# Kernel tuning notes

Measured on AMD Instinct MI355X. Metric: run time of the kernel, lower is better.

Reference implementation:

```python
import jax, jax.numpy as jnp
import numpy as np

B, D, NH, HD, L, P, FF = 2, 256, 8, 32, 4, 4, 1024
SPATIAL = np.array([[100, 100], [50, 50], [25, 25], [13, 13]], dtype=np.int64)
S_TOTAL = int(SPATIAL.prod(1).sum())  # 13294
EPS = 1e-5


def setup_inputs() -> dict:
    key = jax.random.key(0)
    ks = jax.random.split(key, 20)
    std = 0.02
    f32 = jnp.float32
    return {
        "query": jax.random.normal(ks[0], (B, S_TOTAL, D), f32),
        "query_pos": jax.random.normal(ks[1], (B, S_TOTAL, D), f32),
        "valid_ratios": jnp.ones((B, L, 2), f32),
        "spatial_shapes": SPATIAL,
        "level_start_index": np.concatenate([[0], SPATIAL.prod(1).cumsum()[:-1]]).astype(np.int64),
        "W_off": jax.random.normal(ks[2], (D, NH * L * P * 2), f32) * std,
        "b_off": jax.random.normal(ks[3], (NH * L * P * 2,), f32) * std,
        "W_attn": jax.random.normal(ks[4], (D, NH * L * P), f32) * std,
        "b_attn": jax.random.normal(ks[5], (NH * L * P,), f32) * std,
        "W_val": jax.random.normal(ks[6], (D, D), f32) * std,
        "b_val": jnp.zeros((D,), f32),
        "W_out": jax.random.normal(ks[7], (D, D), f32) * std,
        "b_out": jnp.zeros((D,), f32),
        "ln1_g": jnp.ones((D,), f32),
        "ln1_b": jnp.zeros((D,), f32),
        "W1": jax.random.normal(ks[8], (D, FF), f32) * std,
        "b1": jnp.zeros((FF,), f32),
        "W2": jax.random.normal(ks[9], (FF, D), f32) * std,
        "b2": jnp.zeros((D,), f32),
        "ln2_g": jnp.ones((D,), f32),
        "ln2_b": jnp.zeros((D,), f32),
    }


def _layer_norm(x, g, b):
    m = x.mean(-1, keepdims=True)
    v = ((x - m) ** 2).mean(-1, keepdims=True)
    return (x - m) * jax.lax.rsqrt(v + EPS) * g + b


def _bilinear_sample(v, loc, H, W):
    # v: [B, NH, H*W, HD]; loc: [B, NH, S, P, 2] normalized to [0,1]
    # Matches F.grid_sample(bilinear, padding_mode='zeros', align_corners=False)
    x = loc[..., 0] * W - 0.5
    y = loc[..., 1] * H - 0.5
    x0 = jnp.floor(x)
    y0 = jnp.floor(y)
    lx, ly = x - x0, y - y0
    x0i = x0.astype(jnp.int32)
    y0i = y0.astype(jnp.int32)
    x1i, y1i = x0i + 1, y0i + 1

    def corner(yi, xi, w):
        valid = (xi >= 0) & (xi < W) & (yi >= 0) & (yi < H)
        idx = jnp.clip(yi, 0, H - 1) * W + jnp.clip(xi, 0, W - 1)  # [B,NH,S,P]
        b_, h_, s_, p_ = idx.shape
        g = jnp.take_along_axis(v, idx.reshape(b_, h_, s_ * p_)[..., None], axis=2)
        g = g.reshape(b_, h_, s_, p_, -1)
        return g * (w * valid)[..., None]

    return (corner(y0i, x0i, (1 - lx) * (1 - ly)) + corner(y0i, x1i, lx * (1 - ly))
            + corner(y1i, x0i, (1 - lx) * ly) + corner(y1i, x1i, lx * ly))


def _forward(query, query_pos, valid_ratios, spatial_shapes,
             W_off, b_off, W_attn, b_attn, W_val, b_val, W_out, b_out,
             ln1_g, ln1_b, W1, b1, W2, b2, ln2_g, ln2_b):
    ss = np.asarray(spatial_shapes)
    Bq, S, _ = query.shape

    # ----- reference points (per-pixel centers, normalized by valid ratios) -----
    refs = []
    for lvl in range(ss.shape[0]):
        H, W = int(ss[lvl, 0]), int(ss[lvl, 1])
        ry, rx = jnp.meshgrid(jnp.linspace(0.5, H - 0.5, H), jnp.linspace(0.5, W - 0.5, W), indexing='ij')
        vy = valid_ratios[:, lvl, 1][:, None, None]
        vx = valid_ratios[:, lvl, 0][:, None, None]
        ry = ry[None] / (vy * H)
        rx = rx[None] / (vx * W)
        refs.append(jnp.stack((rx, ry), -1).reshape(Bq, H * W, 2))
    ref = jnp.concatenate(refs, 1)  # [B, S, 2] (identical across levels)

    # ----- multi-scale deformable attention -----
    q = query + query_pos
    v = (query @ W_val + b_val).reshape(Bq, S, NH, HD).transpose(0, 2, 1, 3)  # [B,NH,S,HD]
    off = (q @ W_off + b_off).reshape(Bq, S, NH, L, P, 2)
    aw = jax.nn.softmax((q @ W_attn + b_attn).reshape(Bq, S, NH, L * P), -1)
    aw = aw.reshape(Bq, S, NH, L, P)
    normalizer = jnp.asarray(ss[:, ::-1].copy(), jnp.float32)  # (W, H) per level
    loc = ref[:, :, None, None, None, :] + off / normalizer[None, None, None, :, None, :]  # [B,S,NH,L,P,2]

    starts = np.concatenate([[0], ss.prod(1).cumsum()[:-1]])
    out = jnp.zeros((Bq, NH, S, HD), query.dtype)
    for lvl in range(ss.shape[0]):
        H, W = int(ss[lvl, 0]), int(ss[lvl, 1])
        s0 = int(starts[lvl])
        v_l = v[:, :, s0:s0 + H * W]                       # [B,NH,HW,HD]
        loc_l = loc[:, :, :, lvl].transpose(0, 2, 1, 3, 4)  # [B,NH,S,P,2]
        samp = _bilinear_sample(v_l, loc_l, H, W)           # [B,NH,S,P,HD]
        w_l = aw[:, :, :, lvl].transpose(0, 2, 1, 3)        # [B,NH,S,P]
        out = out + (samp * w_l[..., None]).sum(3)
    attn_out = out.transpose(0, 2, 1, 3).reshape(Bq, S, D) @ W_out + b_out

    # ----- residual + LN + FFN + residual + LN -----
    x = _layer_norm(query + attn_out, ln1_g, ln1_b)
    f = jax.nn.relu(x @ W1 + b1) @ W2 + b2
    return _layer_norm(x + f, ln2_g, ln2_b)


def reference(query, query_pos, valid_ratios, spatial_shapes, level_start_index,
              W_off, b_off, W_attn, b_attn, W_val, b_val, W_out, b_out,
              ln1_g, ln1_b, W1, b1, W2, b2, ln2_g, ln2_b):
    return _forward(query, query_pos, valid_ratios, spatial_shapes,
                    W_off, b_off, W_attn, b_attn, W_val, b_val, W_out, b_out,
                    ln1_g, ln1_b, W1, b1, W2, b2, ln2_g, ln2_b)
```

## Files before the change

### kernel.cpp

```cpp
#include <hip/hip_runtime.h>
#include <math.h>

#define R_ROWS 26588
#define S_TOT  13294
#define NHEAD  8
#define NLVL   4
#define EPSF   1e-5f

typedef __attribute__((ext_vector_type(8))) short short8;
typedef __attribute__((ext_vector_type(4))) float f32x4;
typedef __attribute__((ext_vector_type(2))) float f32x2;
typedef unsigned short ushort_t;

__device__ __forceinline__ unsigned short f2bf(float f) {
    unsigned int u = __builtin_bit_cast(unsigned int, f);
    unsigned int r = (u + 0x7FFFu + ((u >> 16) & 1u)) >> 16;
    return (unsigned short)r;
}

__global__ __launch_bounds__(256) void prep_kernel(
    const float* __restrict__ W_val, const float* __restrict__ W_off,
    const float* __restrict__ W_attn, const float* __restrict__ W_out,
    const float* __restrict__ W1, const float* __restrict__ W2,
    ushort_t* __restrict__ wt_val, ushort_t* __restrict__ wt_off,
    ushort_t* __restrict__ wt_attn, ushort_t* __restrict__ wt_out,
    ushort_t* __restrict__ wt_w1, ushort_t* __restrict__ wt_w2,
    const float* __restrict__ query, const float* __restrict__ qpos,
    ushort_t* __restrict__ qry_bf, ushort_t* __restrict__ qsum_bf)
{
    __shared__ ushort_t tt[32][33];
    int bid = blockIdx.x;
    if (bid < 736) {
        const float* src; ushort_t* dst; int K, N, t;
        if (bid < 64)       { src = W_val;  dst = wt_val;  K = 256;  N = 256;  t = bid; }
        else if (bid < 128) { src = W_off;  dst = wt_off;  K = 256;  N = 256;  t = bid - 64; }
        else if (bid < 160) { src = W_attn; dst = wt_attn; K = 256;  N = 128;  t = bid - 128; }
        else if (bid < 224) { src = W_out;  dst = wt_out;  K = 256;  N = 256;  t = bid - 160; }
        else if (bid < 480) { src = W1;     dst = wt_w1;   K = 256;  N = 1024; t = bid - 224; }
        else                { src = W2;     dst = wt_w2;   K = 1024; N = 256;  t = bid - 480; }
        int nt = N / 32;
        int bn = (t % nt) * 32, bk = (t / nt) * 32;
        int x = threadIdx.x & 31;
        int y = threadIdx.x >> 5;
#pragma unroll
        for (int i = 0; i < 4; ++i) {
            int k = y + i * 8;
            tt[x][k] = f2bf(src[(long)(bk + k) * N + bn + x]);
        }
        __syncthreads();
#pragma unroll
        for (int i = 0; i < 4; ++i) {
            int n = y + i * 8;
            dst[(long)(bn + n) * K + bk + x] = tt[n][x];
        }
    } else {
        int i = (bid - 736) * 256 + threadIdx.x;
        float4 a = ((const float4*)query)[i];
        float4 b = ((const float4*)qpos)[i];
        uint2 qa, qs;
        qa.x = (unsigned)f2bf(a.x) | ((unsigned)f2bf(a.y) << 16);
        qa.y = (unsigned)f2bf(a.z) | ((unsigned)f2bf(a.w) << 16);
        qs.x = (unsigned)f2bf(a.x + b.x) | ((unsigned)f2bf(a.y + b.y) << 16);
        qs.y = (unsigned)f2bf(a.z + b.z) | ((unsigned)f2bf(a.w + b.w) << 16);
        ((uint2*)qry_bf)[i] = qa;
        ((uint2*)qsum_bf)[i] = qs;
    }
}

__device__ __forceinline__ void stage_ab(
    const ushort_t* __restrict__ Arow, const ushort_t* __restrict__ Brow,
    int K, int k0, ushort_t* As, ushort_t* Bs, int wave, int lane)
{
    int quadS = lane & 3;
    int rr = lane >> 2;
#pragma unroll
    for (int inst = 0; inst < 2; ++inst) {
        int base_row = wave * 32 + inst * 16;
        int r = base_row + rr;
        int quadG = quadS ^ ((r >> 1) & 3);
        const ushort_t* gp = Arow + (long)r * K + k0 + quadG * 8;
        __builtin_amdgcn_global_load_lds(
            (const __attribute__((address_space(1))) unsigned int*)gp,
            (__attribute__((address_space(3))) unsigned int*)&As[base_row * 32],
            16, 0, 0);
    }
#pragma unroll
    for (int inst = 0; inst < 2; ++inst) {
        int base_row = wave * 32 + inst * 16;
        int r = base_row + rr;
        int quadG = quadS ^ ((r >> 1) & 3);
        const ushort_t* gp = Brow + (long)r * K + k0 + quadG * 8;
        __builtin_amdgcn_global_load_lds(
            (const __attribute__((address_space(1))) unsigned int*)gp,
            (__attribute__((address_space(3))) unsigned int*)&Bs[base_row * 32],
            16, 0, 0);
    }
}

__device__ __forceinline__ void gemm_body(
    ushort_t* As, ushort_t* Bs,
    const ushort_t* __restrict__ A, const ushort_t* __restrict__ Wt,
    const float* __restrict__ bias, void* __restrict__ Cv,
    int M, int N, int K, int bm, int bn, bool out_bf16, bool relu)
{
    const int tid  = threadIdx.x;
    const int wave = tid >> 6;
    const int lane = tid & 63;
    const int l15  = lane & 15;
    const int quad = lane >> 4;
    const int wm   = (wave >> 1) * 64;
    const int wn   = (wave & 1) * 64;

    const ushort_t* Arow = A + (long)bm * K;
    const ushort_t* Brow = Wt + (long)bn * K;

    f32x4 acc[4][4];
#pragma unroll
    for (int i = 0; i < 4; ++i)
#pragma unroll
        for (int j = 0; j < 4; ++j) acc[i][j] = (f32x4)0.0f;

    int aoff[4], boff[4];
#pragma unroll
    for (int mi = 0; mi < 4; ++mi) {
        int r = wm + mi * 16 + l15;
        aoff[mi] = r * 32 + (quad ^ ((r >> 1) & 3)) * 8;
    }
#pragma unroll
    for (int ni = 0; ni < 4; ++ni) {
        int r = wn + ni * 16 + l15;
        boff[ni] = r * 32 + (quad ^ ((r >> 1) & 3)) * 8;
    }

    const int NT = K >> 5;
    stage_ab(Arow, Brow, K, 0,  As,        Bs,        wave, lane);
    stage_ab(Arow, Brow, K, 32, As + 4096, Bs + 4096, wave, lane);
    int cur = 0;
    for (int t = 0; t < NT; ++t) {
        if (t + 2 < NT) {
            int nb = (cur + 2) & 3;
            stage_ab(Arow, Brow, K, (t + 2) << 5,
                     As + nb * 4096, Bs + nb * 4096, wave, lane);
            asm volatile("s_waitcnt vmcnt(8)" ::: "memory");
        } else if (t + 2 == NT) {
            asm volatile("s_waitcnt vmcnt(4)" ::: "memory");
        } else {
            asm volatile("s_waitcnt vmcnt(0)" ::: "memory");
        }
        asm volatile("s_barrier" ::: "memory");

        const ushort_t* Ab = As + cur * 4096;
        const ushort_t* Bb = Bs + cur * 4096;
        short8 af[4], bf[4];
#pragma unroll
        for (int mi = 0; mi < 4; ++mi) af[mi] = *(const short8*)&Ab[aoff[mi]];
#pragma unroll
        for (int ni = 0; ni < 4; ++ni) bf[ni] = *(const short8*)&Bb[boff[ni]];
#pragma unroll
        for (int mi = 0; mi < 4; ++mi)
#pragma unroll
            for (int ni = 0; ni < 4; ++ni)
                acc[mi][ni] = __builtin_amdgcn_mfma_f32_16x16x32_bf16(
                    af[mi], bf[ni], acc[mi][ni], 0, 0, 0);
        cur = (cur + 1) & 3;
    }

#pragma unroll
    for (int mi = 0; mi < 4; ++mi) {
#pragma unroll
        for (int r = 0; r < 4; ++r) {
            int row = bm + wm + mi * 16 + quad * 4 + r;
            if (row >= M) continue;
#pragma unroll
            for (int ni = 0; ni < 4; ++ni) {
                int col = bn + wn + ni * 16 + l15;
                float vv = acc[mi][ni][r] + bias[col];
                if (relu) vv = fmaxf(vv, 0.f);
                if (out_bf16)
                    ((ushort_t*)Cv)[(long)row * N + col] = f2bf(vv);
                else
                    ((float*)Cv)[(long)row * N + col] = vv;
            }
        }
    }
}

template<bool OUT_BF16, bool RELU>
__global__ __launch_bounds__(256) void gemm_mfma_kernel(
    const ushort_t* __restrict__ A, const ushort_t* __restrict__ Wt,
    const float* __restrict__ bias, void* __restrict__ Cv,
    int M, int N, int K)
{
    __shared__ ushort_t As[4 * 4096];
    __shared__ ushort_t Bs[4 * 4096];
    gemm_body(As, Bs, A, Wt, bias, Cv, M, N, K,
              blockIdx.x * 128, blockIdx.y * 128, OUT_BF16, RELU);
}

__global__ __launch_bounds__(256) void proj_kernel(
    const ushort_t* __restrict__ qry_bf, const ushort_t* __restrict__ q_bf,
    const ushort_t* __restrict__ wt_val, const ushort_t* __restrict__ wt_off,
    const ushort_t* __restrict__ wt_attn,
    const float* __restrict__ b_val, const float* __restrict__ b_off,
    const float* __restrict__ b_attn,
    ushort_t* __restrict__ v_bf, float* __restrict__ cb, float* __restrict__ logits)
{
    __shared__ ushort_t As[4 * 4096];
    __shared__ ushort_t Bs[4 * 4096];
    int y = blockIdx.y;
    const ushort_t* A; const ushort_t* Wt; const float* bias;
    void* C; bool outbf; int N, bn;
    if (y < 2)      { A = qry_bf; Wt = wt_val;  bias = b_val;  C = v_bf;   outbf = true;  N = 256; bn = y * 128; }
    else if (y < 4) { A = q_bf;   Wt = wt_off;  bias = b_off;  C = cb;     outbf = false; N = 256; bn = (y - 2) * 128; }
    else            { A = q_bf;   Wt = wt_attn; bias = b_attn; C = logits; outbf = false; N = 128; bn = 0; }
    gemm_body(As, Bs, A, Wt, bias, C, R_ROWS, N, 256, blockIdx.x * 128, bn, outbf, false);
}

__device__ __forceinline__ void stage_ln64(
    const ushort_t* __restrict__ Arow, const ushort_t* __restrict__ Brow,
    int K, int k0, ushort_t* As, ushort_t* Bs, int wave, int lane)
{
    int quadS = lane & 3;
    int rr = lane >> 2;
    {
        int base_row = wave * 16;
        int r = base_row + rr;
        int quadG = quadS ^ ((r >> 1) & 3);
        const ushort_t* gp = Arow + (long)r * K + k0 + quadG * 8;
        __builtin_amdgcn_global_load_lds(
            (const __attribute__((address_space(1))) unsigned int*)gp,
            (__attribute__((address_space(3))) unsigned int*)&As[base_row * 32],
            16, 0, 0);
    }
#pragma unroll
    for (int inst = 0; inst < 4; ++inst) {
        int base_row = wave * 64 + inst * 16;
        int r = base_row + rr;
        int quadG = quadS ^ ((r >> 1) & 3);
        const ushort_t* gp = Brow + (long)r * K + k0 + quadG * 8;
        __builtin_amdgcn_global_load_lds(
            (const __attribute__((address_space(1))) unsigned int*)gp,
            (__attribute__((address_space(3))) unsigned int*)&Bs[base_row * 32],
            16, 0, 0);
    }
}

template<bool DUAL>
__global__ __launch_bounds__(256, 2) void gemm_ln_kernel(
    const ushort_t* __restrict__ A, const ushort_t* __restrict__ Wt,
    const float* __restrict__ bias, const float* __restrict__ resid,
    const float* __restrict__ gam, const float* __restrict__ bet,
    float* __restrict__ outf, ushort_t* __restrict__ outb,
    int M, int K)
{
    __shared__ ushort_t As[3 * 2048];
    __shared__ ushort_t Bs[3 * 8192];
    __shared__ float s1s[64][4], s2s[64][4];

    const int tid  = threadIdx.x;
    const int wave = tid >> 6;
    const int lane = tid & 63;
    const int l15  = lane & 15;
    const int quad = lane >> 4;
    const int wn   = wave * 64;
    const int bm   = blockIdx.x * 64;

    const ushort_t* Arow = A + (long)bm * K;

    float bias4[4], g4[4], be4[4];
#pragma unroll
    for (int ni = 0; ni < 4; ++ni) {
        int col = wn + ni * 16 + l15;
        bias4[ni] = bias[col];
        g4[ni]    = gam[col];
        be4[ni]   = bet[col];
    }
    float rv[4][4][4];
#pragma unroll
    for (int mi = 0; mi < 4; ++mi)
#pragma unroll
        for (int rr = 0; rr < 4; ++rr) {
            int row = bm + mi * 16 + quad * 4 + rr;
#pragma unroll
            for (int ni = 0; ni < 4; ++ni) {
                int col = wn + ni * 16 + l15;
                rv[mi][rr][ni] = (row < M) ? resid[(long)row * 256 + col] : 0.f;
            }
        }

    f32x4 acc[4][4];
#pragma unroll
    for (int i = 0; i < 4; ++i)
#pragma unroll
        for (int j = 0; j < 4; ++j) acc[i][j] = (f32x4)0.0f;

    int aoff[4], boff[4];
#pragma unroll
    for (int mi = 0; mi < 4; ++mi) {
        int r = mi * 16 + l15;
        aoff[mi] = r * 32 + (quad ^ ((r >> 1) & 3)) * 8;
    }
#pragma unroll
    for (int ni = 0; ni < 4; ++ni) {
        int r = wn + ni * 16 + l15;
        boff[ni] = r * 32 + (quad ^ ((r >> 1) & 3)) * 8;
    }

    const int NT = K >> 5;
    stage_ln64(Arow, Wt, K, 0, As, Bs, wave, lane);
    int cur = 0;
    for (int t = 0; t < NT; ++t) {
        int nxt = cur + 1; if (nxt == 3) nxt = 0;
        if (t + 1 < NT) {
            stage_ln64(Arow, Wt, K, (t + 1) << 5,
                       As + nxt * 2048, Bs + nxt * 8192, wave, lane);
            asm volatile("s_waitcnt vmcnt(5)" ::: "memory");
        } else {
            asm volatile("s_waitcnt vmcnt(0)" ::: "memory");
        }
        asm volatile("s_barrier" ::: "memory");

        const ushort_t* Ab = As + cur * 2048;
        const ushort_t* Bb = Bs + cur * 8192;
        short8 af[4], bf[4];
#pragma unroll
        for (int mi = 0; mi < 4; ++mi) af[mi] = *(const short8*)&Ab[aoff[mi]];
#pragma unroll
        for (int ni = 0; ni < 4; ++ni) bf[ni] = *(const short8*)&Bb[boff[ni]];
#pragma unroll
        for (int mi = 0; mi < 4; ++mi)
#pragma unroll
            for (int ni = 0; ni < 4; ++ni)
                acc[mi][ni] = __builtin_amdgcn_mfma_f32_16x16x32_bf16(
                    af[mi], bf[ni], acc[mi][ni], 0, 0, 0);
        cur = nxt;
    }

#pragma unroll
    for (int mi = 0; mi < 4; ++mi)
#pragma unroll
        for (int rr = 0; rr < 4; ++rr) {
            float s1 = 0.f, s2 = 0.f;
#pragma unroll
            for (int ni = 0; ni < 4; ++ni) {
                float x = acc[mi][ni][rr] + bias4[ni] + rv[mi][rr][ni];
                acc[mi][ni][rr] = x;
                s1 += x; s2 += x * x;
            }
#pragma unroll
            for (int o = 1; o < 16; o <<= 1) {
                s1 += __shfl_xor(s1, o);
                s2 += __shfl_xor(s2, o);
            }
            if (l15 == 0) {
                int rl = mi * 16 + quad * 4 + rr;
                s1s[rl][wave] = s1;
                s2s[rl][wave] = s2;
            }
        }
    __syncthreads();
#pragma unroll
    for (int mi = 0; mi < 4; ++mi)
#pragma unroll
        for (int rr = 0; rr < 4; ++rr) {
            int rl  = mi * 16 + quad * 4 + rr;
            int row = bm + rl;
            float t1 = s1s[rl][0] + s1s[rl][1] + s1s[rl][2] + s1s[rl][3];
            float t2 = s2s[rl][0] + s2s[rl][1] + s2s[rl][2] + s2s[rl][3];
            float mean = t1 * (1.f / 256.f);
            float var  = t2 * (1.f / 256.f) - mean * mean;
            float inv  = rsqrtf(var + EPSF);
            if (row < M) {
#pragma unroll
                for (int ni = 0; ni < 4; ++ni) {
                    int col = wn + ni * 16 + l15;
                    float y = (acc[mi][ni][rr] - mean) * inv * g4[ni] + be4[ni];
                    outf[(long)row * 256 + col] = y;
                    if (DUAL) outb[(long)row * 256 + col] = f2bf(y);
                }
            }
        }
}

#define DEF_BLOCKS 3328
#define DEF_CHUNK  416

__global__ __launch_bounds__(256) void deform_sample_kernel(
    const ushort_t* __restrict__ v, const float* __restrict__ off,
    const float* __restrict__ logits, const float* __restrict__ vr,
    ushort_t* __restrict__ out)
{
    const int Hs_[4] = {100, 50, 25, 13};
    const int S0_[4] = {0, 10000, 12500, 13125};

    int wb  = (blockIdx.x & 7) * DEF_CHUNK + (blockIdx.x >> 3);
    int grp = wb * 64 + (threadIdx.x >> 2);
    int j   = threadIdx.x & 3;
    if (grp >= R_ROWS * NHEAD) return;
    int h = grp & 7;
    int r = grp >> 3;
    int b = (r >= S_TOT) ? 1 : 0;
    int s = r - b * S_TOT;

    int lq = (s < 10000) ? 0 : (s < 12500) ? 1 : (s < 13125) ? 2 : 3;
    int t  = s - S0_[lq];
    int Wq = Hs_[lq];
    int iy = t / Wq;
    int jx = t - iy * Wq;
    float vx = vr[(b * NLVL + lq) * 2 + 0];
    float vy = vr[(b * NLVL + lq) * 2 + 1];
    float rx = (jx + 0.5f) / (vx * (float)Wq);
    float ry = (iy + 0.5f) / (vy * (float)Wq);

    const float* offp = off + (long)r * 256 + h * 32;
    float4 oa = ((const float4*)offp)[2 * j];
    float4 ob = ((const float4*)offp)[2 * j + 1];
    float4 lg = ((const float4*)(logits + (long)grp * 16))[j];

    float mx = fmaxf(fmaxf(lg.x, lg.y), fmaxf(lg.z, lg.w));
    mx = fmaxf(mx, __shfl_xor(mx, 1));
    mx = fmaxf(mx, __shfl_xor(mx, 2));
    float e0 = __expf(lg.x - mx), e1 = __expf(lg.y - mx);
    float e2 = __expf(lg.z - mx), e3 = __expf(lg.w - mx);
    float sum = e0 + e1 + e2 + e3;
    sum += __shfl_xor(sum, 1);
    sum += __shfl_xor(sum, 2);
    float inv = 1.f / sum;

    const int   H  = Hs_[j];
    const float fH = (float)H;
    const int   s0 = S0_[j];
    float oxs[4] = {oa.x, oa.z, ob.x, ob.z};
    float oys[4] = {oa.y, oa.w, ob.y, ob.w};
    float wts[4] = {e0 * inv, e1 * inv, e2 * inv, e3 * inv};
    float pw0[4], pw1[4], pw2[4], pw3[4];
    int   pi0[4], pi1[4], pi2[4], pi3[4];
#pragma unroll
    for (int i = 0; i < 4; ++i) {
        float x = rx * fH + oxs[i] - 0.5f;
        float y = ry * fH + oys[i] - 0.5f;
        float xf = floorf(x), yf = floorf(y);
        float lx = x - xf, ly = y - yf;
        int x0 = (int)xf, y0 = (int)yf;
        bool xv0 = (x0 >= 0) & (x0 < H);
        bool xv1 = (x0 >= -1) & (x0 < H - 1);
        bool yv0 = (y0 >= 0) & (y0 < H);
        bool yv1 = (y0 >= -1) & (y0 < H - 1);
        float w = wts[i];
        pw0[i] = (xv0 & yv0) ? (1.f - lx) * (1.f - ly) * w : 0.f;
        pw1[i] = (xv1 & yv0) ? lx * (1.f - ly) * w : 0.f;
        pw2[i] = (xv0 & yv1) ? (1.f - lx) * ly * w : 0.f;
        pw3[i] = (xv1 & yv1) ? lx * ly * w : 0.f;
        int xc0 = min(max(x0, 0), H - 1), xc1 = min(max(x0 + 1, 0), H - 1);
        int yc0 = min(max(y0, 0), H - 1), yc1 = min(max(y0 + 1, 0), H - 1);
        pi0[i] = s0 + yc0 * H + xc0;
        pi1[i] = s0 + yc0 * H + xc1;
        pi2[i] = s0 + yc1 * H + xc0;
        pi3[i] = s0 + yc1 * H + xc1;
    }

    const ushort_t* vb = v + ((long)b * S_TOT) * 256 + h * 32 + j * 8;
    f32x2 acc2[4];
#pragma unroll
    for (int c = 0; c < 4; ++c) acc2[c] = (f32x2)0.0f;

#define ACC_CORNER(IDX, WGT) do {                                            \
        uint4 g = *(const uint4*)&vb[(long)(IDX) * 256];                     \
        unsigned uu0 = g.x, uu1 = g.y, uu2 = g.z, uu3 = g.w;                 \
        f32x2 gv;                                                            \
        gv.x = __builtin_bit_cast(float, uu0 << 16);                         \
        gv.y = __builtin_bit_cast(float, uu0 & 0xFFFF0000u);                 \
        acc2[0] += gv * (WGT);                                               \
        gv.x = __builtin_bit_cast(float, uu1 << 16);                         \
        gv.y = __builtin_bit_cast(float, uu1 & 0xFFFF0000u);                 \
        acc2[1] += gv * (WGT);                                               \
        gv.x = __builtin_bit_cast(float, uu2 << 16);                         \
        gv.y = __builtin_bit_cast(float, uu2 & 0xFFFF0000u);                 \
        acc2[2] += gv * (WGT);                                               \
        gv.x = __builtin_bit_cast(float, uu3 << 16);                         \
        gv.y = __builtin_bit_cast(float, uu3 & 0xFFFF0000u);                 \
        acc2[3] += gv * (WGT);                                               \
    } while (0)

#pragma unroll
    for (int i = 0; i < 4; ++i) {
#pragma unroll
        for (int j2 = 0; j2 < 4; ++j2) {
            float w00 = __shfl(pw0[i], j2, 4);
            float w01 = __shfl(pw1[i], j2, 4);
            float w10 = __shfl(pw2[i], j2, 4);
            float w11 = __shfl(pw3[i], j2, 4);
            int   i00 = __shfl(pi0[i], j2, 4);
            int   i01 = __shfl(pi1[i], j2, 4);
            int   i10 = __shfl(pi2[i], j2, 4);
            int   i11 = __shfl(pi3[i], j2, 4);
            ACC_CORNER(i00, w00);
            ACC_CORNER(i01, w01);
            ACC_CORNER(i10, w10);
            ACC_CORNER(i11, w11);
        }
    }
#undef ACC_CORNER

    uint4 o;
    o.x = (unsigned)f2bf(acc2[0].x) | ((unsigned)f2bf(acc2[0].y) << 16);
    o.y = (unsigned)f2bf(acc2[1].x) | ((unsigned)f2bf(acc2[1].y) << 16);
    o.z = (unsigned)f2bf(acc2[2].x) | ((unsigned)f2bf(acc2[2].y) << 16);
    o.w = (unsigned)f2bf(acc2[3].x) | ((unsigned)f2bf(acc2[3].y) << 16);
    *(uint4*)&out[(long)r * 256 + h * 32 + j * 8] = o;
}

extern "C" void kernel_launch(void* const* d_in, const int* in_sizes, int n_in,
                              void* d_out, int out_size, void* d_ws, size_t ws_size,
                              hipStream_t stream)
{
    const float* query  = (const float*)d_in[0];
    const float* qpos   = (const float*)d_in[1];
    const float* vr     = (const float*)d_in[2];
    const float* W_off  = (const float*)d_in[5];
    const float* b_off  = (const float*)d_in[6];
    const float* W_attn = (const float*)d_in[7];
    const float* b_attn = (const float*)d_in[8];
    const float* W_val  = (const float*)d_in[9];
    const float* b_val  = (const float*)d_in[10];
    const float* W_out  = (const float*)d_in[11];
    const float* b_out  = (const float*)d_in[12];
    const float* ln1g   = (const float*)d_in[13];
    const float* ln1b   = (const float*)d_in[14];
    const float* W1     = (const float*)d_in[15];
    const float* b1     = (const float*)d_in[16];
    const float* W2     = (const float*)d_in[17];
    const float* b2     = (const float*)d_in[18];
    const float* ln2g   = (const float*)d_in[19];
    const float* ln2b   = (const float*)d_in[20];
    float* out = (float*)d_out;

    float* ws = (float*)d_ws;
    const long R128 = (long)R_ROWS * 128;
    ushort_t* q_bf    = (ushort_t*)(ws);
    ushort_t* qry_bf  = (ushort_t*)(ws + R128);
    ushort_t* v_bf    = (ushort_t*)(ws + 2 * R128);
    float*    logits  = ws + 3 * R128;
    ushort_t* h_bf    = (ushort_t*)(ws);
    float*    cb      = ws + 4 * R128;
    ushort_t* samp_bf = (ushort_t*)(ws + 6 * R128);
    float*    xb      = ws + 7 * R128;
    ushort_t* wt      = (ushort_t*)(ws + 9 * R128);
    ushort_t* wt_val  = wt;
    ushort_t* wt_off  = wt + 65536;
    ushort_t* wt_attn = wt + 131072;
    ushort_t* wt_out  = wt + 163840;
    ushort_t* wt_w1   = wt + 229376;
    ushort_t* wt_w2   = wt + 491520;

    dim3 blk(256);
    const int MB128 = (R_ROWS + 127) / 128;
    const int MB64  = (R_ROWS + 63) / 64;

    prep_kernel<<<736 + R_ROWS / 4, blk, 0, stream>>>(
        W_val, W_off, W_attn, W_out, W1, W2,
        wt_val, wt_off, wt_attn, wt_out, wt_w1, wt_w2,
        query, qpos, qry_bf, q_bf);
    proj_kernel<<<dim3(MB128, 5), blk, 0, stream>>>(
        qry_bf, q_bf, wt_val, wt_off, wt_attn, b_val, b_off, b_attn,
        v_bf, cb, logits);
    deform_sample_kernel<<<DEF_BLOCKS, blk, 0, stream>>>(
        v_bf, cb, logits, vr, samp_bf);
    gemm_ln_kernel<true><<<MB64, blk, 0, stream>>>(
        samp_bf, wt_out, b_out, query, ln1g, ln1b, xb, samp_bf, R_ROWS, 256);
    gemm_mfma_kernel<true, true><<<dim3(MB128, 8), blk, 0, stream>>>(
        samp_bf, wt_w1, b1, h_bf, R_ROWS, 1024, 256);
    gemm_ln_kernel<false><<<MB64, blk, 0, stream>>>(
        h_bf, wt_w2, b2, xb, ln2g, ln2b, out, nullptr, R_ROWS, 1024);
}
```

Measured before the change: 316.0 us.

## Stage sampling weights and byte offsets in LDS instead of shuffles, batch gathers

The deformable sampling kernel now writes each group's per-corner weights and precomputed byte offsets into shared memory, rather than broadcasting 128 values per thread with cross-lane shuffles. The gather loop reads two points' metadata with vector LDS loads and issues eight 16-byte gathers before doing the FMAs, which raises memory-level parallelism. Offsets are precomputed as 32-bit byte offsets to avoid 64-bit address math, and launch bounds now request 4 blocks per CU. The cost is about 33KB of LDS per block, which can limit occupancy, and the sync relies on an lgkmcnt wait within a 4-lane group rather than a barrier.

Result: no change. 312.5 us (-1.1%).

```diff
diff --git a/kernel.cpp b/kernel.cpp
--- a/kernel.cpp
+++ b/kernel.cpp
@@ -385,13 +385,15 @@
 #define DEF_BLOCKS 3328
 #define DEF_CHUNK  416
 
-__global__ __launch_bounds__(256) void deform_sample_kernel(
+__global__ __launch_bounds__(256, 4) void deform_sample_kernel(
     const ushort_t* __restrict__ v, const float* __restrict__ off,
     const float* __restrict__ logits, const float* __restrict__ vr,
     ushort_t* __restrict__ out)
 {
     const int Hs_[4] = {100, 50, 25, 13};
     const int S0_[4] = {0, 10000, 12500, 13125};
+
+    __shared__ float meta[64 * 132];
 
     int wb  = (blockIdx.x & 7) * DEF_CHUNK + (blockIdx.x >> 3);
     int grp = wb * 64 + (threadIdx.x >> 2);
@@ -430,11 +432,12 @@
     const int   H  = Hs_[j];
     const float fH = (float)H;
     const int   s0 = S0_[j];
+    const int   boff = b ? (S_TOT * 512) : 0;
     float oxs[4] = {oa.x, oa.z, ob.x, ob.z};
     float oys[4] = {oa.y, oa.w, ob.y, ob.w};
     float wts[4] = {e0 * inv, e1 * inv, e2 * inv, e3 * inv};
-    float pw0[4], pw1[4], pw2[4], pw3[4];
-    int   pi0[4], pi1[4], pi2[4], pi3[4];
+
+    float* mg = &meta[(threadIdx.x >> 2) * 132];
 #pragma unroll
     for (int i = 0; i < 4; ++i) {
         float x = rx * fH + oxs[i] - 0.5f;
@@ -447,26 +450,32 @@
         bool yv0 = (y0 >= 0) & (y0 < H);
         bool yv1 = (y0 >= -1) & (y0 < H - 1);
         float w = wts[i];
-        pw0[i] = (xv0 & yv0) ? (1.f - lx) * (1.f - ly) * w : 0.f;
-        pw1[i] = (xv1 & yv0) ? lx * (1.f - ly) * w : 0.f;
-        pw2[i] = (xv0 & yv1) ? (1.f - lx) * ly * w : 0.f;
-        pw3[i] = (xv1 & yv1) ? lx * ly * w : 0.f;
+        f32x4 w4;
+        w4.x = (xv0 & yv0) ? (1.f - lx) * (1.f - ly) * w : 0.f;
+        w4.y = (xv1 & yv0) ? lx * (1.f - ly) * w : 0.f;
+        w4.z = (xv0 & yv1) ? (1.f - lx) * ly * w : 0.f;
+        w4.w = (xv1 & yv1) ? lx * ly * w : 0.f;
         int xc0 = min(max(x0, 0), H - 1), xc1 = min(max(x0 + 1, 0), H - 1);
         int yc0 = min(max(y0, 0), H - 1), yc1 = min(max(y0 + 1, 0), H - 1);
-        pi0[i] = s0 + yc0 * H + xc0;
-        pi1[i] = s0 + yc0 * H + xc1;
-        pi2[i] = s0 + yc1 * H + xc0;
-        pi3[i] = s0 + yc1 * H + xc1;
-    }
-
-    const ushort_t* vb = v + ((long)b * S_TOT) * 256 + h * 32 + j * 8;
+        int4 o4;
+        o4.x = ((s0 + yc0 * H + xc0) << 9) + boff;
+        o4.y = ((s0 + yc0 * H + xc1) << 9) + boff;
+        o4.z = ((s0 + yc1 * H + xc0) << 9) + boff;
+        o4.w = ((s0 + yc1 * H + xc1) << 9) + boff;
+        int pt = i * 4 + j;
+        *(f32x4*)&mg[pt * 8]     = w4;
+        *(int4*) &mg[pt * 8 + 4] = o4;
+    }
+    asm volatile("s_waitcnt lgkmcnt(0)" ::: "memory");
+
+    const char* vbase = (const char*)v;
+    const unsigned loff = (unsigned)(h * 64 + j * 16);
     f32x2 acc2[4];
 #pragma unroll
     for (int c = 0; c < 4; ++c) acc2[c] = (f32x2)0.0f;
 
-#define ACC_CORNER(IDX, WGT) do {                                            \
-        uint4 g = *(const uint4*)&vb[(long)(IDX) * 256];                     \
-        unsigned uu0 = g.x, uu1 = g.y, uu2 = g.z, uu3 = g.w;                 \
+#define FMA4(G, WGT) do {                                                    \
+        unsigned uu0 = (G).x, uu1 = (G).y, uu2 = (G).z, uu3 = (G).w;         \
         f32x2 gv;                                                            \
         gv.x = __builtin_bit_cast(float, uu0 << 16);                         \
         gv.y = __builtin_bit_cast(float, uu0 & 0xFFFF0000u);                 \
@@ -483,24 +492,23 @@
     } while (0)
 
 #pragma unroll
-    for (int i = 0; i < 4; ++i) {
-#pragma unroll
-        for (int j2 = 0; j2 < 4; ++j2) {
-            float w00 = __shfl(pw0[i], j2, 4);
-            float w01 = __shfl(pw1[i], j2, 4);
-            float w10 = __shfl(pw2[i], j2, 4);
-            float w11 = __shfl(pw3[i], j2, 4);
-            int   i00 = __shfl(pi0[i], j2, 4);
-            int   i01 = __shfl(pi1[i], j2, 4);
-            int   i10 = __shfl(pi2[i], j2, 4);
-            int   i11 = __shfl(pi3[i], j2, 4);
-            ACC_CORNER(i00, w00);
-            ACC_CORNER(i01, w01);
-            ACC_CORNER(i10, w10);
-            ACC_CORNER(i11, w11);
-        }
-    }
-#undef ACC_CORNER
+    for (int pp = 0; pp < 8; ++pp) {
+        f32x4 wA = *(const f32x4*)&mg[(2 * pp) * 8];
+        int4  oA = *(const int4*) &mg[(2 * pp) * 8 + 4];
+        f32x4 wB = *(const f32x4*)&mg[(2 * pp + 1) * 8];
+        int4  oB = *(const int4*) &mg[(2 * pp + 1) * 8 + 4];
+        uint4 gA0 = *(const uint4*)(vbase + ((unsigned)oA.x + loff));
+        uint4 gA1 = *(const uint4*)(vbase + ((unsigned)oA.y + loff));
+        uint4 gA2 = *(const uint4*)(vbase + ((unsigned)oA.z + loff));
+        uint4 gA3 = *(const uint4*)(vbase + ((unsigned)oA.w + loff));
+        uint4 gB0 = *(const uint4*)(vbase + ((unsigned)oB.x + loff));
+        uint4 gB1 = *(const uint4*)(vbase + ((unsigned)oB.y + loff));
+        uint4 gB2 = *(const uint4*)(vbase + ((unsigned)oB.z + loff));
+        uint4 gB3 = *(const uint4*)(vbase + ((unsigned)oB.w + loff));
+        FMA4(gA0, wA.x); FMA4(gA1, wA.y); FMA4(gA2, wA.z); FMA4(gA3, wA.w);
+        FMA4(gB0, wB.x); FMA4(gB1, wB.y); FMA4(gB2, wB.z); FMA4(gB3, wB.w);
+    }
+#undef FMA4
 
     uint4 o;
     o.x = (unsigned)f2bf(acc2[0].x) | ((unsigned)f2bf(acc2[0].y) << 16);
```
